# Optimization experiments

Measured on AMD Instinct MI355X. Metric: run time of the kernel, lower is better.

## Reference

```python
import jax, jax.numpy as jnp
import numpy as np

B, S, E, H = 2, 2048, 2048, 16
D = E // H  # head_dim = 128


def setup_inputs() -> dict:
    key = jax.random.key(0)
    k1, k2, k3, k4, k5 = jax.random.split(key, 5)
    hidden_states = jax.random.normal(k1, (B, S, E), dtype=jnp.float32)
    # causal mask, broadcastable to attn_shape (B, q, H, k)
    causal = jnp.tril(jnp.ones((S, S), dtype=bool))  # [q, k]
    attention_mask = jnp.broadcast_to(causal[None, :, None, :], (B, S, 1, S))
    c_attn_w = jax.random.normal(k2, (E, E + 2 * D), dtype=jnp.float32) * (E ** -0.5)
    c_attn_b = jax.random.normal(k3, (E + 2 * D,), dtype=jnp.float32) * 0.02
    c_proj_w = jax.random.normal(k4, (E, E), dtype=jnp.float32) * (E ** -0.5)
    c_proj_b = jax.random.normal(k5, (E,), dtype=jnp.float32) * 0.02
    return {
        "hidden_states": hidden_states,
        "attention_mask": attention_mask,
        "c_attn_w": c_attn_w,
        "c_attn_b": c_attn_b,
        "c_proj_w": c_proj_w,
        "c_proj_b": c_proj_b,
    }


def reference(hidden_states, attention_mask, c_attn_w, c_attn_b, c_proj_w, c_proj_b):
    b, s, e = hidden_states.shape
    h, d = H, D
    qkv = hidden_states @ c_attn_w + c_attn_b            # [b, s, e + 2d]
    query = qkv[..., :e]                                 # [b, s, e]
    key = qkv[..., e:e + d]                              # [b, s, d] (single shared KV head)
    value = qkv[..., e + d:]                             # [b, s, d]
    scale = 1.0 / (d ** 0.5)                             # scale_attn_weights, unscale=1
    q = query.reshape(b, s * h, d)
    # QK^T with MQA broadcast: [b, s*h, k]
    scores = jnp.einsum('bqd,bkd->bqk', q, key) * scale
    scores = scores.reshape(b, s, h, s)                  # attn_shape (b, q, h, k)
    mask_value = jnp.finfo(scores.dtype).min
    scores = jnp.where(attention_mask, scores, mask_value)
    probs = jax.nn.softmax(scores, axis=-1)              # fp32 softmax (upcast is no-op in fp32)
    attn = jnp.einsum('bqk,bkd->bqd', probs.reshape(b, s * h, s), value)
    attn = attn.reshape(b, s, e)
    return attn @ c_proj_w + c_proj_b
```

## Files before the change

kernel.cpp:

```cpp
#include <hip/hip_runtime.h>
#include <math.h>


typedef __attribute__((ext_vector_type(8))) short short8;
typedef __attribute__((ext_vector_type(8))) __bf16 bf16x8;
typedef __attribute__((ext_vector_type(4))) float floatx4;
typedef __attribute__((ext_vector_type(4))) unsigned short ushort4v;
typedef __attribute__((ext_vector_type(2))) unsigned uint2v;
typedef unsigned short ushort;

__device__ __forceinline__ ushort f2bf(float f) {
    unsigned u = __builtin_bit_cast(unsigned, f);
    u += 0x7fffu + ((u >> 16) & 1u);
    return (ushort)(u >> 16);
}
__device__ __forceinline__ unsigned pk2(float a, float b) {
    return (unsigned)f2bf(a) | ((unsigned)f2bf(b) << 16);
}

template <typename V>
__device__ __forceinline__ auto mfma_try(V a, V b, floatx4 c, int)
    -> decltype(__builtin_amdgcn_mfma_f32_16x16x32_bf16(a, b, c, 0, 0, 0)) {
    return __builtin_amdgcn_mfma_f32_16x16x32_bf16(a, b, c, 0, 0, 0);
}
template <typename V>
__device__ __forceinline__ floatx4 mfma_try(V a, V b, floatx4 c, long) {
    return __builtin_amdgcn_mfma_f32_16x16x32_bf16(
        __builtin_bit_cast(bf16x8, a), __builtin_bit_cast(bf16x8, b), c, 0, 0, 0);
}
__device__ __forceinline__ floatx4 mfma_bf16(short8 a, short8 b, floatx4 c) {
    return mfma_try(a, b, c, 0);
}

__device__ __forceinline__ void gld_lds16(const ushort* g, ushort* l) {
    __builtin_amdgcn_global_load_lds(
        (const __attribute__((address_space(1))) unsigned*)(const void*)g,
        (__attribute__((address_space(3))) unsigned*)(void*)l, 16, 0, 0);
}

__global__ __launch_bounds__(256) void convert_bf16(const float* __restrict__ X,
                                                    ushort* __restrict__ Y, int n4) {
    int i = blockIdx.x * 256 + threadIdx.x;
    if (i >= n4) return;
    float4 v = ((const float4*)X)[i];
    ushort4v o = {f2bf(v.x), f2bf(v.y), f2bf(v.z), f2bf(v.w)};
    *(ushort4v*)&Y[(size_t)i * 4] = o;
}

__global__ __launch_bounds__(256) void transpose_convert(const float* __restrict__ W,
                                                         ushort* __restrict__ WT,
                                                         int K, int N) {
    __shared__ ushort T[64][68];
    const int tid = threadIdx.x;
    const int n0 = blockIdx.x * 64, k0 = blockIdx.y * 64;
    #pragma unroll
    for (int i = 0; i < 4; ++i) {
        int k = (tid >> 4) + i * 16, n = (tid & 15) * 4;
        float4 v = *(const float4*)&W[(size_t)(k0 + k) * N + n0 + n];
        T[n + 0][k] = f2bf(v.x); T[n + 1][k] = f2bf(v.y);
        T[n + 2][k] = f2bf(v.z); T[n + 3][k] = f2bf(v.w);
    }
    __syncthreads();
    #pragma unroll
    for (int i = 0; i < 4; ++i) {
        int idx = tid + i * 256;
        int n = idx >> 4, c4 = idx & 15;
        *(ushort4v*)&WT[(size_t)(n0 + n) * K + k0 + c4 * 4] =
            *(const ushort4v*)&T[n][c4 * 4];
    }
}

__global__ __launch_bounds__(256) void v_transpose(const ushort* __restrict__ qkv,
                                                   ushort* __restrict__ VTg) {
    __shared__ ushort T[64 * 72];
    const int tid = threadIdx.x;
    const int s0 = blockIdx.x * 64, d0 = blockIdx.y * 64, b = blockIdx.z;
    const size_t bS = (size_t)b * 2048;
    #pragma unroll
    for (int i = 0; i < 2; ++i) {
        int idx = tid + i * 256;
        int s = idx >> 3, d8 = idx & 7;
        short8 v = *(const short8*)&qkv[(bS + s0 + s) * 2304 + 2176 + d0 + d8 * 8];
        #pragma unroll
        for (int j = 0; j < 8; ++j)
            T[(d8 * 8 + j) * 72 + s] = (ushort)v[j];
    }
    __syncthreads();
    #pragma unroll
    for (int i = 0; i < 2; ++i) {
        int idx = tid + i * 256;
        int d = idx >> 3, s8 = idx & 7;
        *(short8*)&VTg[((size_t)b * 128 + d0 + d) * 2048 + s0 + s8 * 8] =
            *(const short8*)&T[d * 72 + s8 * 8];
    }
}

template <int MODE>
__global__ __launch_bounds__(256) void gemm_m97(
    const ushort* __restrict__ A, const ushort* __restrict__ BT,
    const float* __restrict__ bias, void* __restrict__ C, int M, int N, int K)
{
    __shared__ ushort As[8192];
    __shared__ ushort Bs[8192];
    const int tid = threadIdx.x, lane = tid & 63, wid = tid >> 6;
    const int wr = wid >> 1, wc = wid & 1;
    const int lg = lane >> 4, li = lane & 15;
    const int m0 = blockIdx.y * 128, n0 = blockIdx.x * 128;
    const int srow = lane >> 3;
    const int sphys = (lane & 7) * 16;
    floatx4 acc[4][4] = {};

    for (int k0 = 0; k0 < K; k0 += 64) {
        __syncthreads();
        #pragma unroll
        for (int i = 0; i < 4; ++i) {
            const int c = wid * 4 + i;
            const int row = c * 8 + srow;
            const int lin = sphys ^ ((row & 7) << 4);
            gld_lds16(&A[(size_t)(m0 + row) * K + k0 + (lin >> 1)], &As[c * 512]);
            gld_lds16(&BT[(size_t)(n0 + row) * K + k0 + (lin >> 1)], &Bs[c * 512]);
        }
        __syncthreads();
        #pragma unroll
        for (int kk = 0; kk < 2; ++kk) {
            short8 af[4], bfv[4];
            const int pb = (kk * 64 + lg * 16) ^ ((li & 7) << 4);
            #pragma unroll
            for (int m = 0; m < 4; ++m)
                af[m] = *(const short8*)&As[(wr * 64 + m * 16 + li) * 64 + (pb >> 1)];
            #pragma unroll
            for (int n = 0; n < 4; ++n)
                bfv[n] = *(const short8*)&Bs[(wc * 64 + n * 16 + li) * 64 + (pb >> 1)];
            #pragma unroll
            for (int m = 0; m < 4; ++m)
                #pragma unroll
                for (int n = 0; n < 4; ++n)
                    acc[m][n] = mfma_bf16(af[m], bfv[n], acc[m][n]);
        }
    }

    #pragma unroll
    for (int m = 0; m < 4; ++m) {
        #pragma unroll
        for (int n = 0; n < 4; ++n) {
            const int col = n0 + wc * 64 + n * 16 + li;
            const float bv = bias[col];
            #pragma unroll
            for (int r = 0; r < 4; ++r) {
                const int row = m0 + wr * 64 + m * 16 + lg * 4 + r;
                float v = acc[m][n][r] + bv;
                if constexpr (MODE == 0) {
                    if (col < 2048) v *= 0.08838834764831845f;
                    ((ushort*)C)[(size_t)row * N + col] = f2bf(v);
                } else {
                    ((float*)C)[(size_t)row * N + col] = v;
                }
            }
        }
    }
}

#define STAGE_KV(t_, Kdst, Vdst)                                               \
    {                                                                          \
        const int k0_ = (t_) * 64;                                             \
        _Pragma("unroll")                                                      \
        for (int i_ = 0; i_ < 4; ++i_) {                                       \
            const int idx_ = tid + i_ * 256;                                   \
            const int row_ = idx_ >> 4, g_ = idx_ & 15;                        \
            const int src_ = (g_ * 16) ^ ((row_ & 7) << 4);                    \
            gld_lds16(&qkv[(bS + k0_ + row_) * QKV + E + (src_ >> 1)],         \
                      &(Kdst)[(i_ * 256 + wid * 64) * 8]);                     \
        }                                                                      \
        _Pragma("unroll")                                                      \
        for (int i_ = 0; i_ < 4; ++i_) {                                       \
            const int idx_ = tid + i_ * 256;                                   \
            const int d_ = idx_ >> 3, kg_ = idx_ & 7;                          \
            gld_lds16(&VTg[((size_t)b * 128 + d_) * 2048 + k0_ +               \
                           ((kg_ ^ (d_ & 7)) << 3)],                           \
                      &(Vdst)[(i_ * 256 + wid * 64) * 8]);                     \
        }                                                                      \
    }

__global__ __launch_bounds__(256, 2) void attn_kernel(
    const ushort* __restrict__ qkv,
    const ushort* __restrict__ VTg,
    ushort* __restrict__ out)
{
    constexpr int S = 2048, Dh = 128, QKV = 2304, E = 2048;
    __shared__ ushort lds[40960];
    ushort* Ks0 = lds;
    ushort* Ks1 = lds + 8192;
    ushort* VT0 = lds + 16384;
    ushort* VT1 = lds + 24576;
    ushort* Ps  = lds + 32768;

    const int tid = threadIdx.x, lane = tid & 63, wid = tid >> 6;
    const int lg = lane >> 4, li = lane & 15;
    const int pr = blockIdx.x;
    const int h = blockIdx.y, b = blockIdx.z;
    const size_t bS = (size_t)b * S;

    for (int pass = 0; pass < 2; ++pass) {
        const int st = pass ? (15 - pr) : pr;
        const int qA = st * 128 + wid * 16;
        const int qB = qA + 64;

        short8 qfA[4], qfB[4];
        #pragma unroll
        for (int dc = 0; dc < 4; ++dc) {
            qfA[dc] = *(const short8*)&qkv[(bS + qA + li) * QKV + h * Dh + dc * 32 + lg * 8];
            qfB[dc] = *(const short8*)&qkv[(bS + qB + li) * QKV + h * Dh + dc * 32 + lg * 8];
        }

        floatx4 oA[8] = {}, oB[8] = {};
        float mA = -1e30f, lA = 0.f, mB = -1e30f, lB = 0.f;
        const int ntiles = 2 * st + 2;

        STAGE_KV(0, Ks0, VT0);

        for (int t = 0; t < ntiles; ++t) {
            __builtin_amdgcn_s_barrier();
            ushort* Kcur = (t & 1) ? Ks1 : Ks0;
            ushort* Vcur = (t & 1) ? VT1 : VT0;
            if (t + 1 < ntiles) {
                ushort* Knxt = (t & 1) ? Ks0 : Ks1;
                ushort* Vnxt = (t & 1) ? VT0 : VT1;
                STAGE_KV(t + 1, Knxt, Vnxt);
                asm volatile("s_waitcnt vmcnt(8)" ::: "memory");
            } else {
                asm volatile("s_waitcnt vmcnt(0)" ::: "memory");
            }
            __builtin_amdgcn_sched_barrier(0);
            __builtin_amdgcn_s_barrier();

            floatx4 sA[4] = {{0,0,0,0},{0,0,0,0},{0,0,0,0},{0,0,0,0}};
            floatx4 sB[4] = {{0,0,0,0},{0,0,0,0},{0,0,0,0},{0,0,0,0}};
            __builtin_amdgcn_s_setprio(1);
            #pragma unroll
            for (int dc = 0; dc < 4; ++dc) {
                #pragma unroll
                for (int kb = 0; kb < 4; ++kb) {
                    short8 kf = *(const short8*)&Kcur[(kb * 16 + li) * 128 +
                                                      (((dc * 4 + lg) ^ (li & 7)) << 3)];
                    sA[kb] = mfma_bf16(kf, qfA[dc], sA[kb]);
                    sB[kb] = mfma_bf16(kf, qfB[dc], sB[kb]);
                }
            }
            __builtin_amdgcn_s_setprio(0);

            if (t == 2 * st) {
                #pragma unroll
                for (int kb = 0; kb < 4; ++kb)
                    #pragma unroll
                    for (int r = 0; r < 4; ++r)
                        if (kb * 16 + lg * 4 + r > wid * 16 + li) sA[kb][r] = -1e30f;
            }
            if (t == 2 * st + 1) {
                #pragma unroll
                for (int kb = 0; kb < 4; ++kb)
                    #pragma unroll
                    for (int r = 0; r < 4; ++r) {
                        sA[kb][r] = -1e30f;
                        if (kb * 16 + lg * 4 + r > wid * 16 + li) sB[kb][r] = -1e30f;
                    }
            }

            {
                float mt = fmaxf(fmaxf(fmaxf(sA[0][0], sA[0][1]), fmaxf(sA[0][2], sA[0][3])),
                                 fmaxf(fmaxf(sA[1][0], sA[1][1]), fmaxf(sA[1][2], sA[1][3])));
                mt = fmaxf(mt, fmaxf(fmaxf(fmaxf(sA[2][0], sA[2][1]), fmaxf(sA[2][2], sA[2][3])),
                                     fmaxf(fmaxf(sA[3][0], sA[3][1]), fmaxf(sA[3][2], sA[3][3]))));
                mt = fmaxf(mt, __shfl_xor(mt, 16));
                mt = fmaxf(mt, __shfl_xor(mt, 32));
                if (!__all(mt <= mA)) {
                    const float mn = fmaxf(mA, mt);
                    const float sc = __expf(mA - mn);
                    mA = mn;
                    lA *= sc;
                    #pragma unroll
                    for (int db = 0; db < 8; ++db) oA[db] *= sc;
                }
                float rs = 0.f;
                #pragma unroll
                for (int kb = 0; kb < 4; ++kb)
                    #pragma unroll
                    for (int r = 0; r < 4; ++r) {
                        float p = __expf(sA[kb][r] - mA);
                        sA[kb][r] = p; rs += p;
                    }
                rs += __shfl_xor(rs, 16);
                rs += __shfl_xor(rs, 32);
                lA += rs;
                #pragma unroll
                for (int kb = 0; kb < 4; ++kb) {
                    const int g = kb * 2 + (lg >> 1);
                    const int sw = ((g ^ (li & 7)) << 3) + ((lg & 1) * 4);
                    uint2v w = {pk2(sA[kb][0], sA[kb][1]), pk2(sA[kb][2], sA[kb][3])};
                    *(uint2v*)&Ps[wid * 2048 + li * 64 + sw] = w;
                }
            }
            {
                float mt = fmaxf(fmaxf(fmaxf(sB[0][0], sB[0][1]), fmaxf(sB[0][2], sB[0][3])),
                                 fmaxf(fmaxf(sB[1][0], sB[1][1]), fmaxf(sB[1][2], sB[1][3])));
                mt = fmaxf(mt, fmaxf(fmaxf(fmaxf(sB[2][0], sB[2][1]), fmaxf(sB[2][2], sB[2][3])),
                                     fmaxf(fmaxf(sB[3][0], sB[3][1]), fmaxf(sB[3][2], sB[3][3]))));
                mt = fmaxf(mt, __shfl_xor(mt, 16));
                mt = fmaxf(mt, __shfl_xor(mt, 32));
                if (!__all(mt <= mB)) {
                    const float mn = fmaxf(mB, mt);
                    const float sc = __expf(mB - mn);
                    mB = mn;
                    lB *= sc;
                    #pragma unroll
                    for (int db = 0; db < 8; ++db) oB[db] *= sc;
                }
                float rs = 0.f;
                #pragma unroll
                for (int kb = 0; kb < 4; ++kb)
                    #pragma unroll
                    for (int r = 0; r < 4; ++r) {
                        float p = __expf(sB[kb][r] - mB);
                        sB[kb][r] = p; rs += p;
                    }
                rs += __shfl_xor(rs, 16);
                rs += __shfl_xor(rs, 32);
                lB += rs;
                #pragma unroll
                for (int kb = 0; kb < 4; ++kb) {
                    const int g = kb * 2 + (lg >> 1);
                    const int sw = ((g ^ (li & 7)) << 3) + ((lg & 1) * 4);
                    uint2v w = {pk2(sB[kb][0], sB[kb][1]), pk2(sB[kb][2], sB[kb][3])};
                    *(uint2v*)&Ps[wid * 2048 + 1024 + li * 64 + sw] = w;
                }
            }

            __builtin_amdgcn_s_setprio(1);
            #pragma unroll
            for (int kc = 0; kc < 2; ++kc) {
                short8 pA = *(const short8*)&Ps[wid * 2048 + li * 64 +
                                                (((kc * 4 + lg) ^ (li & 7)) << 3)];
                short8 pB = *(const short8*)&Ps[wid * 2048 + 1024 + li * 64 +
                                                (((kc * 4 + lg) ^ (li & 7)) << 3)];
                #pragma unroll
                for (int db = 0; db < 8; ++db) {
                    short8 vt = *(const short8*)&Vcur[(db * 16 + li) * 64 +
                                                      (((kc * 4 + lg) ^ (li & 7)) << 3)];
                    oA[db] = mfma_bf16(vt, pA, oA[db]);
                    oB[db] = mfma_bf16(vt, pB, oB[db]);
                }
            }
            __builtin_amdgcn_s_setprio(0);
        }

        __syncthreads();
        ushort* Pw = lds + wid * 2176;
        {
            const float inv = 1.0f / lA;
            #pragma unroll
            for (int db = 0; db < 8; ++db) {
                *(unsigned*)&Pw[li * 136 + db * 16 + lg * 4]     = pk2(oA[db][0] * inv, oA[db][1] * inv);
                *(unsigned*)&Pw[li * 136 + db * 16 + lg * 4 + 2] = pk2(oA[db][2] * inv, oA[db][3] * inv);
            }
            #pragma unroll
            for (int i = 0; i < 4; ++i) {
                const int q = lane >> 2, d8 = (lane & 3) + i * 4;
                short8 vv = *(const short8*)&Pw[q * 136 + d8 * 8];
                *(short8*)&out[(bS + qA + q) * E + h * Dh + d8 * 8] = vv;
            }
        }
        {
            const float inv = 1.0f / lB;
            #pragma unroll
            for (int db = 0; db < 8; ++db) {
                *(unsigned*)&Pw[li * 136 + db * 16 + lg * 4]     = pk2(oB[db][0] * inv, oB[db][1] * inv);
                *(unsigned*)&Pw[li * 136 + db * 16 + lg * 4 + 2] = pk2(oB[db][2] * inv, oB[db][3] * inv);
            }
            #pragma unroll
            for (int i = 0; i < 4; ++i) {
                const int q = lane >> 2, d8 = (lane & 3) + i * 4;
                short8 vv = *(const short8*)&Pw[q * 136 + d8 * 8];
                *(short8*)&out[(bS + qB + q) * E + h * Dh + d8 * 8] = vv;
            }
        }
        __syncthreads();
    }
}

extern "C" void kernel_launch(void* const* d_in, const int* in_sizes, int n_in,
                              void* d_out, int out_size, void* d_ws, size_t ws_size,
                              hipStream_t stream) {
    (void)in_sizes; (void)n_in; (void)out_size; (void)ws_size;
    const float* hidden   = (const float*)d_in[0];
    const float* c_attn_w = (const float*)d_in[2];
    const float* c_attn_b = (const float*)d_in[3];
    const float* c_proj_w = (const float*)d_in[4];
    const float* c_proj_b = (const float*)d_in[5];
    float* outp = (float*)d_out;

    char* ws = (char*)d_ws;
    ushort* hbf  = (ushort*)ws;
    ushort* W1T  = (ushort*)(ws + (size_t)16777216);
    ushort* W2T  = (ushort*)(ws + (size_t)16777216 + 9437184);
    ushort* qkv  = (ushort*)(ws + (size_t)16777216 + 9437184 + 8388608);
    ushort* VTg  = (ushort*)(ws + (size_t)16777216 + 9437184 + 8388608 + 18874368);
    ushort* attn = hbf;

    convert_bf16<<<8192, 256, 0, stream>>>(hidden, hbf, 4096 * 2048 / 4);
    transpose_convert<<<dim3(36, 32), 256, 0, stream>>>(c_attn_w, W1T, 2048, 2304);
    transpose_convert<<<dim3(32, 32), 256, 0, stream>>>(c_proj_w, W2T, 2048, 2048);

    gemm_m97<0><<<dim3(18, 32), 256, 0, stream>>>(hbf, W1T, c_attn_b, qkv, 4096, 2304, 2048);
    v_transpose<<<dim3(32, 2, 2), 256, 0, stream>>>(qkv, VTg);
    attn_kernel<<<dim3(8, 16, 2), 256, 0, stream>>>(qkv, VTg, attn);
    gemm_m97<1><<<dim3(16, 32), 256, 0, stream>>>(attn, W2T, c_proj_b, outp, 4096, 2048, 2048);
}
```

Before: 224.2 us.

## Split attention KV loop across two wave groups and merge partial softmax states

The attention block grows to 512 threads arranged as two groups of four waves. Each group processes half of the causal KV tiles with its own double-buffered LDS staging. The partial outputs, running max and running sum from group 1 go through LDS and are merged into group 0's state by log-sum-exp rescaling before the normalized write. This doubles the waves per CU to hide latency and shortens the serial KV loop per query tile. In exchange it needs twice the LDS (now 160KB per block), extra barriers and a merge pass, and the causal masking constant was changed.

```diff
diff --git a/kernel.cpp b/kernel.cpp
--- a/kernel.cpp
+++ b/kernel.cpp
@@ -165,36 +165,34 @@
         const int k0_ = (t_) * 64;                                             \
         _Pragma("unroll")                                                      \
         for (int i_ = 0; i_ < 4; ++i_) {                                       \
-            const int idx_ = tid + i_ * 256;                                   \
+            const int idx_ = gtid + i_ * 256;                                  \
             const int row_ = idx_ >> 4, g_ = idx_ & 15;                        \
             const int src_ = (g_ * 16) ^ ((row_ & 7) << 4);                    \
             gld_lds16(&qkv[(bS + k0_ + row_) * QKV + E + (src_ >> 1)],         \
-                      &(Kdst)[(i_ * 256 + wid * 64) * 8]);                     \
+                      &(Kdst)[(i_ * 256 + gwid * 64) * 8]);                    \
         }                                                                      \
         _Pragma("unroll")                                                      \
         for (int i_ = 0; i_ < 4; ++i_) {                                       \
-            const int idx_ = tid + i_ * 256;                                   \
+            const int idx_ = gtid + i_ * 256;                                  \
             const int d_ = idx_ >> 3, kg_ = idx_ & 7;                          \
             gld_lds16(&VTg[((size_t)b * 128 + d_) * 2048 + k0_ +               \
                            ((kg_ ^ (d_ & 7)) << 3)],                           \
-                      &(Vdst)[(i_ * 256 + wid * 64) * 8]);                     \
+                      &(Vdst)[(i_ * 256 + gwid * 64) * 8]);                    \
         }                                                                      \
     }
 
-__global__ __launch_bounds__(256, 2) void attn_kernel(
+__global__ __launch_bounds__(512, 2) void attn_kernel(
     const ushort* __restrict__ qkv,
     const ushort* __restrict__ VTg,
     ushort* __restrict__ out)
 {
     constexpr int S = 2048, Dh = 128, QKV = 2304, E = 2048;
-    __shared__ ushort lds[40960];
-    ushort* Ks0 = lds;
-    ushort* Ks1 = lds + 8192;
-    ushort* VT0 = lds + 16384;
-    ushort* VT1 = lds + 24576;
-    ushort* Ps  = lds + 32768;
+    __shared__ ushort lds[81920];
+    ushort* Ps = lds + 65536;
 
     const int tid = threadIdx.x, lane = tid & 63, wid = tid >> 6;
+    const int gtid = tid & 255;
+    const int grp = wid >> 2, gwid = wid & 3;
     const int lg = lane >> 4, li = lane & 15;
     const int pr = blockIdx.x;
     const int h = blockIdx.y, b = blockIdx.z;
@@ -202,8 +200,10 @@
 
     for (int pass = 0; pass < 2; ++pass) {
         const int st = pass ? (15 - pr) : pr;
-        const int qA = st * 128 + wid * 16;
+        const int qA = st * 128 + gwid * 16;
         const int qB = qA + 64;
+        const int niter = st + 1;
+        const int tbase = grp * niter;
 
         short8 qfA[4], qfB[4];
         #pragma unroll
@@ -214,18 +214,17 @@
 
         floatx4 oA[8] = {}, oB[8] = {};
         float mA = -1e30f, lA = 0.f, mB = -1e30f, lB = 0.f;
-        const int ntiles = 2 * st + 2;
-
-        STAGE_KV(0, Ks0, VT0);
-
-        for (int t = 0; t < ntiles; ++t) {
+
+        STAGE_KV(tbase, lds + (grp * 2) * 8192, lds + 32768 + (grp * 2) * 8192);
+
+        for (int it = 0; it < niter; ++it) {
+            const int t = tbase + it;
             __builtin_amdgcn_s_barrier();
-            ushort* Kcur = (t & 1) ? Ks1 : Ks0;
-            ushort* Vcur = (t & 1) ? VT1 : VT0;
-            if (t + 1 < ntiles) {
-                ushort* Knxt = (t & 1) ? Ks0 : Ks1;
-                ushort* Vnxt = (t & 1) ? VT0 : VT1;
-                STAGE_KV(t + 1, Knxt, Vnxt);
+            ushort* Kcur = lds + (grp * 2 + (it & 1)) * 8192;
+            ushort* Vcur = lds + 32768 + (grp * 2 + (it & 1)) * 8192;
+            if (it + 1 < niter) {
+                STAGE_KV(t + 1, lds + (grp * 2 + ((it + 1) & 1)) * 8192,
+                         lds + 32768 + (grp * 2 + ((it + 1) & 1)) * 8192);
                 asm volatile("s_waitcnt vmcnt(8)" ::: "memory");
             } else {
                 asm volatile("s_waitcnt vmcnt(0)" ::: "memory");
@@ -253,15 +252,15 @@
                 for (int kb = 0; kb < 4; ++kb)
                     #pragma unroll
                     for (int r = 0; r < 4; ++r)
-                        if (kb * 16 + lg * 4 + r > wid * 16 + li) sA[kb][r] = -1e30f;
+                        if (kb * 16 + lg * 4 + r > gwid * 16 + li) sA[kb][r] = -2e30f;
             }
             if (t == 2 * st + 1) {
                 #pragma unroll
                 for (int kb = 0; kb < 4; ++kb)
                     #pragma unroll
                     for (int r = 0; r < 4; ++r) {
-                        sA[kb][r] = -1e30f;
-                        if (kb * 16 + lg * 4 + r > wid * 16 + li) sB[kb][r] = -1e30f;
+                        sA[kb][r] = -2e30f;
+                        if (kb * 16 + lg * 4 + r > gwid * 16 + li) sB[kb][r] = -2e30f;
                     }
             }
 
@@ -352,9 +351,31 @@
             __builtin_amdgcn_s_setprio(0);
         }
 
-        __syncthreads();
+        float* fbuf = (float*)lds;
         ushort* Pw = lds + wid * 2176;
-        {
+        __syncthreads();
+
+        if (grp == 1) {
+            float* dst = fbuf + (gwid * 64 + lane) * 36;
+            #pragma unroll
+            for (int db = 0; db < 8; ++db) *(floatx4*)&dst[db * 4] = oA[db];
+            dst[32] = mA; dst[33] = lA;
+        }
+        __syncthreads();
+        if (grp == 0) {
+            const float* src = fbuf + (gwid * 64 + lane) * 36;
+            const float m1 = src[32], l1 = src[33];
+            const float mm = fmaxf(mA, m1);
+            const float s0 = __expf(mA - mm), s1 = __expf(m1 - mm);
+            #pragma unroll
+            for (int db = 0; db < 8; ++db) {
+                floatx4 o1 = *(const floatx4*)&src[db * 4];
+                oA[db] = oA[db] * s0 + o1 * s1;
+            }
+            lA = lA * s0 + l1 * s1;
+        }
+        __syncthreads();
+        if (grp == 0) {
             const float inv = 1.0f / lA;
             #pragma unroll
             for (int db = 0; db < 8; ++db) {
@@ -368,7 +389,29 @@
                 *(short8*)&out[(bS + qA + q) * E + h * Dh + d8 * 8] = vv;
             }
         }
-        {
+        __syncthreads();
+
+        if (grp == 1) {
+            float* dst = fbuf + (gwid * 64 + lane) * 36;
+            #pragma unroll
+            for (int db = 0; db < 8; ++db) *(floatx4*)&dst[db * 4] = oB[db];
+            dst[32] = mB; dst[33] = lB;
+        }
+        __syncthreads();
+        if (grp == 0) {
+            const float* src = fbuf + (gwid * 64 + lane) * 36;
+            const float m1 = src[32], l1 = src[33];
+            const float mm = fmaxf(mB, m1);
+            const float s0 = __expf(mB - mm), s1 = __expf(m1 - mm);
+            #pragma unroll
+            for (int db = 0; db < 8; ++db) {
+                floatx4 o1 = *(const floatx4*)&src[db * 4];
+                oB[db] = oB[db] * s0 + o1 * s1;
+            }
+            lB = lB * s0 + l1 * s1;
+        }
+        __syncthreads();
+        if (grp == 0) {
             const float inv = 1.0f / lB;
             #pragma unroll
             for (int db = 0; db < 8; ++db) {
@@ -411,6 +454,6 @@
 
     gemm_m97<0><<<dim3(18, 32), 256, 0, stream>>>(hbf, W1T, c_attn_b, qkv, 4096, 2304, 2048);
     v_transpose<<<dim3(32, 2, 2), 256, 0, stream>>>(qkv, VTg);
-    attn_kernel<<<dim3(8, 16, 2), 256, 0, stream>>>(qkv, VTg, attn);
+    attn_kernel<<<dim3(8, 16, 2), 512, 0, stream>>>(qkv, VTg, attn);
     gemm_m97<1><<<dim3(16, 32), 256, 0, stream>>>(attn, W2T, c_proj_b, outp, 4096, 2048, 2048);
 }
```

Result: faster. 209.5 us (-6.6%).
